# Kernel tuning notes

Hardware: AMD Instinct MI355X
Metric: run time of the kernel (lower is better)

Reference implementation:

```python
import math
import jax, jax.numpy as jnp
import numpy as np

GROUPS = 8

def setup_inputs() -> dict:
    key = jax.random.key(0)
    ks = jax.random.split(key, 6)
    N, H, W, C = 8, 128, 128, 512
    s = 1.0 / math.sqrt(C)
    return {
        "x": jax.random.normal(ks[0], (N, H, W, C), dtype=jnp.float32),
        "Wq": jax.random.normal(ks[1], (C, C), dtype=jnp.float32) * s,
        "Wk": jax.random.normal(ks[2], (C, C), dtype=jnp.float32) * s,
        "Wv": jax.random.normal(ks[3], (C, C), dtype=jnp.float32) * s,
        "Wo": jax.random.normal(ks[4], (C, C), dtype=jnp.float32) * s,
        "bo": jnp.zeros((C,), dtype=jnp.float32),
    }

def reference(x, Wq, Wk, Wv, Wo, bo):
    # width=False: attend along H axis -> permute to [N, W, H, C]
    x = jnp.transpose(x, (0, 2, 1, 3))
    N, W, H, C = x.shape
    g = GROUPS
    gp = C // g  # group_planes (head dim)
    xr = x.reshape(N * W, H, C)
    # torch nn.Linear: y = x @ W^T
    q = (xr @ Wq.T).reshape(N * W, H, g, gp)
    k = (xr @ Wk.T).reshape(N * W, H, g, gp)
    v = (xr @ Wv.T).reshape(N * W, H, g, gp)
    attn = jnp.einsum('nigc,njgc->nijg', q, k / math.sqrt(gp))
    attn = jax.nn.softmax(attn, axis=2)
    out = jnp.einsum('nijg,njgc->nigc', attn, v)
    out = out.reshape(N * W, H, C)
    out = out @ Wo.T + bo
    out = out.reshape(N, W, H, C)
    return jnp.transpose(out, (0, 2, 1, 3))
```

## Files before the change

kernel.cpp:

```cpp
#include <hip/hip_runtime.h>
#include <stdint.h>


#define QKV_LD 1536

typedef __attribute__((ext_vector_type(4))) float f32x4;
typedef __attribute__((ext_vector_type(8))) short bf16x8;
typedef unsigned short u16;
typedef unsigned int u32;

#define CBAR() asm volatile("" ::: "memory")
#define SBAR() do { CBAR(); __builtin_amdgcn_s_barrier(); CBAR(); } while(0)
#define LGKM0() do { asm volatile("s_waitcnt lgkmcnt(0)" ::: "memory"); __builtin_amdgcn_sched_barrier(0); } while(0)
#define VMC(n) asm volatile("s_waitcnt vmcnt(" #n ")" ::: "memory")

static __device__ __forceinline__ u16 f2bf(float f){
    union { float f; u32 u; } v; v.f = f;
    u32 r = v.u + 0x7fffu + ((v.u >> 16) & 1u);
    return (u16)(r >> 16);
}

static __device__ __forceinline__ void gload16(const void* g, void* l){
    __builtin_amdgcn_global_load_lds((const __attribute__((address_space(1))) void*)g,
                                     (__attribute__((address_space(3))) void*)l, 16, 0, 0);
}

__global__ void k_wconv(const float* __restrict__ Wq, const float* __restrict__ Wk,
                        const float* __restrict__ Wv, const float* __restrict__ Wo,
                        u16* __restrict__ Wcat, u16* __restrict__ Wob){
    int e = (blockIdx.x * 256 + threadIdx.x) * 4;
    if (e < 1536*512) {
        int row = e >> 9, col = e & 511;
        const float* s = (row < 512) ? (Wq + row*512)
                        : (row < 1024 ? Wk + (row-512)*512 : Wv + (row-1024)*512);
        float4 v = *(const float4*)(s + col);
        ushort4 o = { f2bf(v.x), f2bf(v.y), f2bf(v.z), f2bf(v.w) };
        *(ushort4*)(Wcat + e) = o;
    } else {
        int e2 = e - 1536*512;
        float4 v = *(const float4*)(Wo + e2);
        ushort4 o = { f2bf(v.x), f2bf(v.y), f2bf(v.z), f2bf(v.w) };
        *(ushort4*)(Wob + e2) = o;
    }
}

__global__ void k_xconv(const float* __restrict__ x, u16* __restrict__ xb, int n0){
    int t = blockIdx.x * 256 + threadIdx.x;
    int ml = t >> 6;
    int c0 = (t & 63) << 3;
    int nl = ml >> 7, h = ml & 127;
    int n = n0 + nl, nb = n >> 7, w = n & 127;
    const float* src = x + (size_t)((nb*128 + h)*128 + w) * 512 + c0;
    float4 a = *(const float4*)(src);
    float4 b = *(const float4*)(src + 4);
    uint4 o;
    o.x = (u32)f2bf(a.x) | ((u32)f2bf(a.y) << 16);
    o.y = (u32)f2bf(a.z) | ((u32)f2bf(a.w) << 16);
    o.z = (u32)f2bf(b.x) | ((u32)f2bf(b.y) << 16);
    o.w = (u32)f2bf(b.z) | ((u32)f2bf(b.w) << 16);
    *(uint4*)(xb + (size_t)ml*512 + c0) = o;
}

template<int LDA, int NCOL, bool OUTPROJ>
__global__ __launch_bounds__(512, 2) void k_gemm2(const u16* __restrict__ A, const u16* __restrict__ B,
                                                  void* __restrict__ Cout, const float* __restrict__ bias,
                                                  int n0, int nrow){
    extern __shared__ char smc[];
    const int tid = threadIdx.x;
    const int wid = tid >> 6, lane = tid & 63, lg = lane >> 4, li = lane & 15;
    const int wm = wid >> 2, wn = wid & 3;
    const int bid = blockIdx.x;
    const int xcd = bid & 7, l = bid >> 3;
    const int row_tile = xcd * (nrow >> 3) + l / NCOL;
    const int col_tile = l % NCOL;
    const int m0 = row_tile * 256, nn0 = col_tile * 256;

    auto stage = [&](const u16* __restrict__ G, int gbase, int kbase, int ld, char* slab){
        #pragma unroll
        for (int i = 0; i < 2; ++i) {
            int R = wid*32 + i*16;
            int r = R + (lane >> 2);
            int srcq = (lane & 3) ^ ((r >> 1) & 3);
            gload16((const char*)(G + (size_t)(gbase + r)*ld + kbase) + srcq*16,
                    slab + R*64);
        }
    };

    f32x4 acc[8][4];
    #pragma unroll
    for (int i = 0; i < 8; ++i)
        #pragma unroll
        for (int j = 0; j < 4; ++j)
            acc[i][j] = f32x4{0.f, 0.f, 0.f, 0.f};

    stage(A, m0, 0,  LDA, smc + 0*16384);
    stage(B, nn0, 0, 512, smc + 1*16384);
    stage(A, m0, 32, LDA, smc + 2*16384);
    stage(B, nn0, 32, 512, smc + 3*16384);
    VMC(4);
    SBAR();

    const int nT = 8;
    int cur = 0;
    bf16x8 af[4], bfr[4];

    for (int t = 0; t < nT; ++t) {
        const bool pf = (t + 1 < nT);
        char* bc = smc + cur*65536;
        char* bn = smc + (cur^1)*65536;
        const int kn = (t + 1) * 64;

        #pragma unroll
        for (int f = 0; f < 4; ++f) {
            int r = wm*128 + f*16 + li;
            af[f] = *(const bf16x8*)(bc + 0*16384 + r*64 + (((lg ^ (r>>1)) & 3) << 4));
        }
        #pragma unroll
        for (int f = 0; f < 4; ++f) {
            int r = wn*64 + f*16 + li;
            bfr[f] = *(const bf16x8*)(bc + 1*16384 + r*64 + (((lg ^ (r>>1)) & 3) << 4));
        }
        if (pf) stage(A, m0, kn, LDA, bn + 0*16384);
        SBAR(); LGKM0();
        __builtin_amdgcn_s_setprio(1);
        #pragma unroll
        for (int f = 0; f < 4; ++f)
            #pragma unroll
            for (int n = 0; n < 4; ++n)
                acc[f][n] = __builtin_amdgcn_mfma_f32_16x16x32_bf16(af[f], bfr[n], acc[f][n], 0, 0, 0);
        __builtin_amdgcn_s_setprio(0);
        SBAR();

        #pragma unroll
        for (int f = 0; f < 4; ++f) {
            int r = wm*128 + (4+f)*16 + li;
            af[f] = *(const bf16x8*)(bc + 0*16384 + r*64 + (((lg ^ (r>>1)) & 3) << 4));
        }
        if (pf) stage(B, nn0, kn, 512, bn + 1*16384);
        if (pf) { VMC(4); } else { VMC(0); }
        SBAR(); LGKM0();
        __builtin_amdgcn_s_setprio(1);
        #pragma unroll
        for (int f = 0; f < 4; ++f)
            #pragma unroll
            for (int n = 0; n < 4; ++n)
                acc[4+f][n] = __builtin_amdgcn_mfma_f32_16x16x32_bf16(af[f], bfr[n], acc[4+f][n], 0, 0, 0);
        __builtin_amdgcn_s_setprio(0);
        SBAR();

        #pragma unroll
        for (int f = 0; f < 4; ++f) {
            int r = wm*128 + f*16 + li;
            af[f] = *(const bf16x8*)(bc + 2*16384 + r*64 + (((lg ^ (r>>1)) & 3) << 4));
        }
        #pragma unroll
        for (int f = 0; f < 4; ++f) {
            int r = wn*64 + f*16 + li;
            bfr[f] = *(const bf16x8*)(bc + 3*16384 + r*64 + (((lg ^ (r>>1)) & 3) << 4));
        }
        if (pf) stage(A, m0, kn + 32, LDA, bn + 2*16384);
        SBAR(); LGKM0();
        __builtin_amdgcn_s_setprio(1);
        #pragma unroll
        for (int f = 0; f < 4; ++f)
            #pragma unroll
            for (int n = 0; n < 4; ++n)
                acc[f][n] = __builtin_amdgcn_mfma_f32_16x16x32_bf16(af[f], bfr[n], acc[f][n], 0, 0, 0);
        __builtin_amdgcn_s_setprio(0);
        SBAR();

        #pragma unroll
        for (int f = 0; f < 4; ++f) {
            int r = wm*128 + (4+f)*16 + li;
            af[f] = *(const bf16x8*)(bc + 2*16384 + r*64 + (((lg ^ (r>>1)) & 3) << 4));
        }
        if (pf) stage(B, nn0, kn + 32, 512, bn + 3*16384);
        if (pf) { VMC(4); }
        SBAR(); LGKM0();
        __builtin_amdgcn_s_setprio(1);
        #pragma unroll
        for (int f = 0; f < 4; ++f)
            #pragma unroll
            for (int n = 0; n < 4; ++n)
                acc[4+f][n] = __builtin_amdgcn_mfma_f32_16x16x32_bf16(af[f], bfr[n], acc[4+f][n], 0, 0, 0);
        __builtin_amdgcn_s_setprio(0);
        SBAR();

        cur ^= 1;
    }

    if (!OUTPROJ) {
        u16* C = (u16*)Cout;
        #pragma unroll
        for (int mf = 0; mf < 8; ++mf)
            #pragma unroll
            for (int nf = 0; nf < 4; ++nf)
                #pragma unroll
                for (int r = 0; r < 4; ++r) {
                    int row = m0 + wm*128 + mf*16 + lg*4 + r;
                    int col = nn0 + wn*64 + nf*16 + li;
                    C[(size_t)row*QKV_LD + col] = f2bf(acc[mf][nf][r]);
                }
    } else {
        float* C = (float*)Cout;
        #pragma unroll
        for (int mf = 0; mf < 8; ++mf)
            #pragma unroll
            for (int nf = 0; nf < 4; ++nf)
                #pragma unroll
                for (int r = 0; r < 4; ++r) {
                    int row = m0 + wm*128 + mf*16 + lg*4 + r;
                    int col = nn0 + wn*64 + nf*16 + li;
                    int mg = n0*128 + row;
                    int n = mg >> 7, ii = mg & 127;
                    int nb = n >> 7, w = n & 127;
                    C[(size_t)((nb*128 + ii)*128 + w) * 512 + col] = acc[mf][nf][r] + bias[col];
                }
    }
}

__global__ __launch_bounds__(256, 2) void k_attn(u16* __restrict__ QKV){
    __shared__ char sm[52224];
    const int g = blockIdx.x;
    const int nl = blockIdx.y;
    const int tid = threadIdx.x;
    const int wid = tid >> 6, lane = tid & 63, lg = lane >> 4, li = lane & 15;

    u16* Qg = QKV + (size_t)nl*128*QKV_LD + g*64;

    #pragma unroll
    for (int it = 0; it < 4; ++it) {
        int gi = it*256 + tid;
        int row = gi >> 3, gs = gi & 7;
        int sw = (gs ^ (row & 7)) << 4;
        gload16((const char*)(Qg + (size_t)row*QKV_LD) + sw,        sm + it*4096 + wid*1024);
        gload16((const char*)(Qg + 512 + (size_t)row*QKV_LD) + sw,  sm + 16384 + it*4096 + wid*1024);
    }
    {
        int j = tid & 127, ch = tid >> 7;
        const u16* src = Qg + 1024 + (size_t)j*QKV_LD + ch*32;
        uint4 a0 = *(const uint4*)(src);
        uint4 a1 = *(const uint4*)(src + 8);
        uint4 a2 = *(const uint4*)(src + 16);
        uint4 a3 = *(const uint4*)(src + 24);
        u32 w[16] = {a0.x,a0.y,a0.z,a0.w, a1.x,a1.y,a1.z,a1.w,
                     a2.x,a2.y,a2.z,a2.w, a3.x,a3.y,a3.z,a3.w};
        char* dst = sm + 34816 + ch*32*272 + j*2;
        #pragma unroll
        for (int cc = 0; cc < 32; ++cc) {
            u32 word = w[cc >> 1];
            u16 val = (cc & 1) ? (u16)(word >> 16) : (u16)(word & 0xffffu);
            *(u16*)(dst + cc*272) = val;
        }
    }
    __syncthreads();

    const int i0w = wid*32;
    f32x4 s[2][8];
    #pragma unroll
    for (int t = 0; t < 2; ++t)
        #pragma unroll
        for (int tj = 0; tj < 8; ++tj)
            s[t][tj] = f32x4{0.f,0.f,0.f,0.f};

    #pragma unroll
    for (int ks = 0; ks < 2; ++ks) {
        bf16x8 qf[2];
        #pragma unroll
        for (int t = 0; t < 2; ++t) {
            int ra = i0w + t*16 + li;
            qf[t] = *(const bf16x8*)(sm + ra*128 + ((ks*64 + lg*16) ^ ((ra & 7) << 4)));
        }
        #pragma unroll
        for (int tj = 0; tj < 8; ++tj) {
            int rb = tj*16 + li;
            bf16x8 kf = *(const bf16x8*)(sm + 16384 + rb*128 + ((ks*64 + lg*16) ^ ((rb & 7) << 4)));
            #pragma unroll
            for (int t = 0; t < 2; ++t)
                s[t][tj] = __builtin_amdgcn_mfma_f32_16x16x32_bf16(qf[t], kf, s[t][tj], 0, 0, 0);
        }
    }
    __syncthreads();

    char* pb = sm + wid*8704;
    #pragma unroll
    for (int t = 0; t < 2; ++t) {
        #pragma unroll
        for (int r = 0; r < 4; ++r) {
            float mx = -1e30f;
            #pragma unroll
            for (int tj = 0; tj < 8; ++tj) mx = fmaxf(mx, s[t][tj][r]);
            #pragma unroll
            for (int off = 1; off < 16; off <<= 1) mx = fmaxf(mx, __shfl_xor(mx, off, 64));
            float p[8]; float sum = 0.f;
            #pragma unroll
            for (int tj = 0; tj < 8; ++tj) { p[tj] = __expf((s[t][tj][r] - mx)*0.125f); sum += p[tj]; }
            #pragma unroll
            for (int off = 1; off < 16; off <<= 1) sum += __shfl_xor(sum, off, 64);
            float inv = 1.0f / sum;
            int prow = t*16 + lg*4 + r;
            #pragma unroll
            for (int tj = 0; tj < 8; ++tj)
                *(u16*)(pb + prow*272 + (tj*16 + li)*2) = f2bf(p[tj]*inv);
        }
    }

    f32x4 o[2][4];
    #pragma unroll
    for (int t = 0; t < 2; ++t)
        #pragma unroll
        for (int tc = 0; tc < 4; ++tc)
            o[t][tc] = f32x4{0.f,0.f,0.f,0.f};

    #pragma unroll
    for (int ks = 0; ks < 4; ++ks) {
        bf16x8 pf[2];
        #pragma unroll
        for (int t = 0; t < 2; ++t)
            pf[t] = *(const bf16x8*)(pb + (t*16 + li)*272 + (ks*64 + lg*16));
        #pragma unroll
        for (int tc = 0; tc < 4; ++tc) {
            bf16x8 vf = *(const bf16x8*)(sm + 34816 + (tc*16 + li)*272 + (ks*64 + lg*16));
            #pragma unroll
            for (int t = 0; t < 2; ++t)
                o[t][tc] = __builtin_amdgcn_mfma_f32_16x16x32_bf16(pf[t], vf, o[t][tc], 0, 0, 0);
        }
    }

    #pragma unroll
    for (int t = 0; t < 2; ++t)
        #pragma unroll
        for (int tc = 0; tc < 4; ++tc)
            #pragma unroll
            for (int r = 0; r < 4; ++r) {
                int irow = i0w + t*16 + lg*4 + r;
                int col = tc*16 + li;
                Qg[(size_t)irow*QKV_LD + col] = f2bf(o[t][tc][r]);
            }
}

extern "C" void kernel_launch(void* const* d_in, const int* in_sizes, int n_in,
                              void* d_out, int out_size, void* d_ws, size_t ws_size,
                              hipStream_t stream){
    const float* x  = (const float*)d_in[0];
    const float* Wq = (const float*)d_in[1];
    const float* Wk = (const float*)d_in[2];
    const float* Wv = (const float*)d_in[3];
    const float* Wo = (const float*)d_in[4];
    const float* bo = (const float*)d_in[5];

    char* ws = (char*)d_ws;
    u16* Wcat = (u16*)ws;
    u16* Wob  = Wcat + 1536*512;

    int CN = 1024;
    while (CN > 64 && (size_t)2097152 + (size_t)CN*524288 > ws_size) CN >>= 1;
    u16* xb  = (u16*)(ws + 2097152);
    u16* QKV = xb + (size_t)CN*128*512;

    hipFuncSetAttribute((const void*)&k_gemm2<512, 6, false>,
                        hipFuncAttributeMaxDynamicSharedMemorySize, 131072);
    hipFuncSetAttribute((const void*)&k_gemm2<QKV_LD, 2, true>,
                        hipFuncAttributeMaxDynamicSharedMemorySize, 131072);

    k_wconv<<<1024, 256, 0, stream>>>(Wq, Wk, Wv, Wo, Wcat, Wob);
    int nch = 1024 / CN;
    for (int ch = 0; ch < nch; ++ch) {
        int n0 = ch * CN;
        int nrow = (CN * 128) / 256;
        k_xconv<<<CN*32, 256, 0, stream>>>(x, xb, n0);
        k_gemm2<512,    6, false><<<nrow*6, 512, 131072, stream>>>(xb, Wcat, QKV, nullptr, 0, nrow);
        k_attn<<<dim3(8, CN), 256, 0, stream>>>(QKV);
        k_gemm2<QKV_LD, 2, true ><<<nrow*2, 512, 131072, stream>>>(QKV, Wob, d_out, bo, n0, nrow);
    }
}
```

Measured before the change: 626.3 us.

## Fuse fp32-to-bf16 input conversion and transpose into QKV GEMM A-tile loading

Removes the separate x conversion kernel and its bf16 staging buffer. The QKV GEMM now loads fp32 x rows directly into registers, converts them to bf16 and writes them to LDS, overlapping this with the MFMA phases. It also drops the LDS XOR swizzle on both A and B tiles and reorders the prefetch/wait schedule. In exchange, the GEMM reads twice the A bytes (fp32, six times over for the column tiles), uses more registers, and may see more LDS bank conflicts without the swizzle.

```diff
diff --git a/kernel.cpp b/kernel.cpp
--- a/kernel.cpp
+++ b/kernel.cpp
@@ -12,6 +12,7 @@
 #define CBAR() asm volatile("" ::: "memory")
 #define SBAR() do { CBAR(); __builtin_amdgcn_s_barrier(); CBAR(); } while(0)
 #define LGKM0() do { asm volatile("s_waitcnt lgkmcnt(0)" ::: "memory"); __builtin_amdgcn_sched_barrier(0); } while(0)
+#define LGKMW() asm volatile("s_waitcnt lgkmcnt(0)" ::: "memory")
 #define VMC(n) asm volatile("s_waitcnt vmcnt(" #n ")" ::: "memory")
 
 static __device__ __forceinline__ u16 f2bf(float f){
@@ -44,25 +45,9 @@
     }
 }
 
-__global__ void k_xconv(const float* __restrict__ x, u16* __restrict__ xb, int n0){
-    int t = blockIdx.x * 256 + threadIdx.x;
-    int ml = t >> 6;
-    int c0 = (t & 63) << 3;
-    int nl = ml >> 7, h = ml & 127;
-    int n = n0 + nl, nb = n >> 7, w = n & 127;
-    const float* src = x + (size_t)((nb*128 + h)*128 + w) * 512 + c0;
-    float4 a = *(const float4*)(src);
-    float4 b = *(const float4*)(src + 4);
-    uint4 o;
-    o.x = (u32)f2bf(a.x) | ((u32)f2bf(a.y) << 16);
-    o.y = (u32)f2bf(a.z) | ((u32)f2bf(a.w) << 16);
-    o.z = (u32)f2bf(b.x) | ((u32)f2bf(b.y) << 16);
-    o.w = (u32)f2bf(b.z) | ((u32)f2bf(b.w) << 16);
-    *(uint4*)(xb + (size_t)ml*512 + c0) = o;
-}
-
-template<int LDA, int NCOL, bool OUTPROJ>
-__global__ __launch_bounds__(512, 2) void k_gemm2(const u16* __restrict__ A, const u16* __restrict__ B,
+template<bool XA, int NCOL, bool OUTPROJ>
+__global__ __launch_bounds__(512, 2) void k_gemm2(const float* __restrict__ X,
+                                                  const u16* __restrict__ A, const u16* __restrict__ B,
                                                   void* __restrict__ Cout, const float* __restrict__ bias,
                                                   int n0, int nrow){
     extern __shared__ char smc[];
@@ -75,15 +60,43 @@
     const int col_tile = l % NCOL;
     const int m0 = row_tile * 256, nn0 = col_tile * 256;
 
-    auto stage = [&](const u16* __restrict__ G, int gbase, int kbase, int ld, char* slab){
+    auto stageG = [&](const u16* __restrict__ G, int gbase, int kb, int ld, char* slab){
         #pragma unroll
         for (int i = 0; i < 2; ++i) {
             int R = wid*32 + i*16;
-            int r = R + (lane >> 2);
-            int srcq = (lane & 3) ^ ((r >> 1) & 3);
-            gload16((const char*)(G + (size_t)(gbase + r)*ld + kbase) + srcq*16,
+            gload16((const char*)(G + (size_t)(gbase + R + (lane >> 2))*ld + kb) + (lane & 3)*16,
                     slab + R*64);
         }
+    };
+
+    const float* xsrc = nullptr;
+    char* adst_off = nullptr;
+    if (XA) {
+        int tokL = m0 + wid*32 + (lane >> 1);
+        int mg = n0*128 + tokL;
+        int n = mg >> 7, h = mg & 127;
+        int nb = n >> 7, w = n & 127;
+        xsrc = X + (size_t)((nb*128 + h)*128 + w)*512 + (lane & 1)*16;
+        adst_off = (char*)(size_t)((wid*32 + (lane >> 1))*64 + (lane & 1)*32);
+    }
+    f32x4 AL0[4], AL1[4];
+    auto loadA = [&](int kb, f32x4* L){
+        #pragma unroll
+        for (int i = 0; i < 4; ++i) L[i] = *(const f32x4*)(xsrc + kb + i*4);
+    };
+    auto writeA = [&](char* slab, const f32x4* L){
+        char* d = slab + (size_t)adst_off;
+        uint4 w0, w1;
+        w0.x = (u32)f2bf(L[0][0]) | ((u32)f2bf(L[0][1]) << 16);
+        w0.y = (u32)f2bf(L[0][2]) | ((u32)f2bf(L[0][3]) << 16);
+        w0.z = (u32)f2bf(L[1][0]) | ((u32)f2bf(L[1][1]) << 16);
+        w0.w = (u32)f2bf(L[1][2]) | ((u32)f2bf(L[1][3]) << 16);
+        w1.x = (u32)f2bf(L[2][0]) | ((u32)f2bf(L[2][1]) << 16);
+        w1.y = (u32)f2bf(L[2][2]) | ((u32)f2bf(L[2][3]) << 16);
+        w1.z = (u32)f2bf(L[3][0]) | ((u32)f2bf(L[3][1]) << 16);
+        w1.w = (u32)f2bf(L[3][2]) | ((u32)f2bf(L[3][3]) << 16);
+        *(uint4*)d = w0;
+        *(uint4*)(d + 16) = w1;
     };
 
     f32x4 acc[8][4];
@@ -93,16 +106,46 @@
         for (int j = 0; j < 4; ++j)
             acc[i][j] = f32x4{0.f, 0.f, 0.f, 0.f};
 
-    stage(A, m0, 0,  LDA, smc + 0*16384);
-    stage(B, nn0, 0, 512, smc + 1*16384);
-    stage(A, m0, 32, LDA, smc + 2*16384);
-    stage(B, nn0, 32, 512, smc + 3*16384);
-    VMC(4);
+    if (XA) {
+        loadA(0, AL0);
+        stageG(B, nn0, 0, 512, smc + 1*16384);
+        loadA(32, AL1);
+        stageG(B, nn0, 32, 512, smc + 3*16384);
+        VMC(8);  writeA(smc + 0*16384, AL0);
+        VMC(2);  writeA(smc + 2*16384, AL1);
+        VMC(0);
+        LGKMW();
+    } else {
+        stageG(A, m0, 0,  QKV_LD, smc + 0*16384);
+        stageG(B, nn0, 0,  512,   smc + 1*16384);
+        stageG(A, m0, 32, QKV_LD, smc + 2*16384);
+        stageG(B, nn0, 32, 512,   smc + 3*16384);
+        VMC(0);
+    }
     SBAR();
 
     const int nT = 8;
     int cur = 0;
     bf16x8 af[4], bfr[4];
+
+    #define RD_A(koff, fbase) \
+        _Pragma("unroll") \
+        for (int f = 0; f < 4; ++f) { \
+            int r = wm*128 + (fbase + f)*16 + li; \
+            af[f] = *(const bf16x8*)(bc + (koff)*16384 + r*64 + (lg << 4)); \
+        }
+    #define RD_B(koff) \
+        _Pragma("unroll") \
+        for (int f = 0; f < 4; ++f) { \
+            int r = wn*64 + f*16 + li; \
+            bfr[f] = *(const bf16x8*)(bc + (koff)*16384 + r*64 + (lg << 4)); \
+        }
+    #define MFMA4x4(abase) \
+        _Pragma("unroll") \
+        for (int f = 0; f < 4; ++f) \
+            _Pragma("unroll") \
+            for (int n = 0; n < 4; ++n) \
+                acc[abase + f][n] = __builtin_amdgcn_mfma_f32_16x16x32_bf16(af[f], bfr[n], acc[abase + f][n], 0, 0, 0);
 
     for (int t = 0; t < nT; ++t) {
         const bool pf = (t + 1 < nT);
@@ -110,84 +153,58 @@
         char* bn = smc + (cur^1)*65536;
         const int kn = (t + 1) * 64;
 
-        #pragma unroll
-        for (int f = 0; f < 4; ++f) {
-            int r = wm*128 + f*16 + li;
-            af[f] = *(const bf16x8*)(bc + 0*16384 + r*64 + (((lg ^ (r>>1)) & 3) << 4));
-        }
-        #pragma unroll
-        for (int f = 0; f < 4; ++f) {
-            int r = wn*64 + f*16 + li;
-            bfr[f] = *(const bf16x8*)(bc + 1*16384 + r*64 + (((lg ^ (r>>1)) & 3) << 4));
-        }
-        if (pf) stage(A, m0, kn, LDA, bn + 0*16384);
+        RD_A(0, 0); RD_B(1);
+        if (pf) {
+            if (XA) loadA(kn, AL0); else stageG(A, m0, kn, QKV_LD, bn + 0*16384);
+            stageG(B, nn0, kn, 512, bn + 1*16384);
+        }
         SBAR(); LGKM0();
         __builtin_amdgcn_s_setprio(1);
-        #pragma unroll
-        for (int f = 0; f < 4; ++f)
-            #pragma unroll
-            for (int n = 0; n < 4; ++n)
-                acc[f][n] = __builtin_amdgcn_mfma_f32_16x16x32_bf16(af[f], bfr[n], acc[f][n], 0, 0, 0);
+        MFMA4x4(0);
         __builtin_amdgcn_s_setprio(0);
         SBAR();
 
-        #pragma unroll
-        for (int f = 0; f < 4; ++f) {
-            int r = wm*128 + (4+f)*16 + li;
-            af[f] = *(const bf16x8*)(bc + 0*16384 + r*64 + (((lg ^ (r>>1)) & 3) << 4));
-        }
-        if (pf) stage(B, nn0, kn, 512, bn + 1*16384);
-        if (pf) { VMC(4); } else { VMC(0); }
+        RD_A(0, 4);
+        if (pf) {
+            if (XA) loadA(kn + 32, AL1); else stageG(A, m0, kn + 32, QKV_LD, bn + 2*16384);
+            stageG(B, nn0, kn + 32, 512, bn + 3*16384);
+        }
         SBAR(); LGKM0();
         __builtin_amdgcn_s_setprio(1);
-        #pragma unroll
-        for (int f = 0; f < 4; ++f)
-            #pragma unroll
-            for (int n = 0; n < 4; ++n)
-                acc[4+f][n] = __builtin_amdgcn_mfma_f32_16x16x32_bf16(af[f], bfr[n], acc[4+f][n], 0, 0, 0);
+        MFMA4x4(4);
+        __builtin_amdgcn_s_setprio(0);
+        if (XA) {
+            if (pf) { VMC(8); writeA(bn + 0*16384, AL0); LGKMW(); }
+            else    { VMC(0); }
+        } else {
+            if (pf) { VMC(4); } else { VMC(0); }
+        }
+        SBAR();
+
+        RD_A(2, 0); RD_B(3);
+        SBAR(); LGKM0();
+        __builtin_amdgcn_s_setprio(1);
+        MFMA4x4(0);
         __builtin_amdgcn_s_setprio(0);
         SBAR();
 
-        #pragma unroll
-        for (int f = 0; f < 4; ++f) {
-            int r = wm*128 + f*16 + li;
-            af[f] = *(const bf16x8*)(bc + 2*16384 + r*64 + (((lg ^ (r>>1)) & 3) << 4));
-        }
-        #pragma unroll
-        for (int f = 0; f < 4; ++f) {
-            int r = wn*64 + f*16 + li;
-            bfr[f] = *(const bf16x8*)(bc + 3*16384 + r*64 + (((lg ^ (r>>1)) & 3) << 4));
-        }
-        if (pf) stage(A, m0, kn + 32, LDA, bn + 2*16384);
+        RD_A(2, 4);
         SBAR(); LGKM0();
         __builtin_amdgcn_s_setprio(1);
-        #pragma unroll
-        for (int f = 0; f < 4; ++f)
-            #pragma unroll
-            for (int n = 0; n < 4; ++n)
-                acc[f][n] = __builtin_amdgcn_mfma_f32_16x16x32_bf16(af[f], bfr[n], acc[f][n], 0, 0, 0);
+        MFMA4x4(4);
         __builtin_amdgcn_s_setprio(0);
+        if (XA) {
+            if (pf) { VMC(2); writeA(bn + 2*16384, AL1); LGKMW(); }
+        } else {
+            if (pf) { VMC(4); }
+        }
         SBAR();
 
-        #pragma unroll
-        for (int f = 0; f < 4; ++f) {
-            int r = wm*128 + (4+f)*16 + li;
-            af[f] = *(const bf16x8*)(bc + 2*16384 + r*64 + (((lg ^ (r>>1)) & 3) << 4));
-        }
-        if (pf) stage(B, nn0, kn + 32, 512, bn + 3*16384);
-        if (pf) { VMC(4); }
-        SBAR(); LGKM0();
-        __builtin_amdgcn_s_setprio(1);
-        #pragma unroll
-        for (int f = 0; f < 4; ++f)
-            #pragma unroll
-            for (int n = 0; n < 4; ++n)
-                acc[4+f][n] = __builtin_amdgcn_mfma_f32_16x16x32_bf16(af[f], bfr[n], acc[4+f][n], 0, 0, 0);
-        __builtin_amdgcn_s_setprio(0);
-        SBAR();
-
         cur ^= 1;
     }
+    #undef RD_A
+    #undef RD_B
+    #undef MFMA4x4
 
     if (!OUTPROJ) {
         u16* C = (u16*)Cout;
@@ -354,13 +371,12 @@
     u16* Wob  = Wcat + 1536*512;
 
     int CN = 1024;
-    while (CN > 64 && (size_t)2097152 + (size_t)CN*524288 > ws_size) CN >>= 1;
-    u16* xb  = (u16*)(ws + 2097152);
-    u16* QKV = xb + (size_t)CN*128*512;
-
-    hipFuncSetAttribute((const void*)&k_gemm2<512, 6, false>,
+    while (CN > 64 && (size_t)2097152 + (size_t)CN*393216 > ws_size) CN >>= 1;
+    u16* QKV = (u16*)(ws + 2097152);
+
+    hipFuncSetAttribute((const void*)&k_gemm2<true, 6, false>,
                         hipFuncAttributeMaxDynamicSharedMemorySize, 131072);
-    hipFuncSetAttribute((const void*)&k_gemm2<QKV_LD, 2, true>,
+    hipFuncSetAttribute((const void*)&k_gemm2<false, 2, true>,
                         hipFuncAttributeMaxDynamicSharedMemorySize, 131072);
 
     k_wconv<<<1024, 256, 0, stream>>>(Wq, Wk, Wv, Wo, Wcat, Wob);
@@ -368,9 +384,8 @@
     for (int ch = 0; ch < nch; ++ch) {
         int n0 = ch * CN;
         int nrow = (CN * 128) / 256;
-        k_xconv<<<CN*32, 256, 0, stream>>>(x, xb, n0);
-        k_gemm2<512,    6, false><<<nrow*6, 512, 131072, stream>>>(xb, Wcat, QKV, nullptr, 0, nrow);
+        k_gemm2<true,  6, false><<<nrow*6, 512, 131072, stream>>>(x, nullptr, Wcat, QKV, nullptr, n0, nrow);
         k_attn<<<dim3(8, CN), 256, 0, stream>>>(QKV);
-        k_gemm2<QKV_LD, 2, true ><<<nrow*2, 512, 131072, stream>>>(QKV, Wob, d_out, bo, n0, nrow);
-    }
-}
+        k_gemm2<false, 2, true ><<<nrow*2, 512, 131072, stream>>>(nullptr, QKV, Wob, d_out, bo, n0, nrow);
+    }
+}
```

After: 731.2 us. 16.7% more time.
